# Kernel tuning notes

Hardware: AMD Instinct MI355X
Metric: run time of the kernel (lower is better)

## Reference

```python
import jax, jax.numpy as jnp
import numpy as np

N = 100000
E = 1000000
HID = 64
EDGE_DIM = 32
N_STEPS = 4


def _gru_cell(x, h, W_ih, b_ih, W_hh, b_hh):
    # PyTorch GRUCell: gates ordered (r, z, n) along the 3*hidden axis
    gi = x @ W_ih.T + b_ih  # [N, 3H]
    gh = h @ W_hh.T + b_hh  # [N, 3H]
    i_r, i_z, i_n = jnp.split(gi, 3, axis=-1)
    h_r, h_z, h_n = jnp.split(gh, 3, axis=-1)
    r = jax.nn.sigmoid(i_r + h_r)
    z = jax.nn.sigmoid(i_z + h_z)
    n = jnp.tanh(i_n + r * h_n)
    return (1.0 - z) * n + z * h


def setup_inputs() -> dict:
    key = jax.random.key(0)
    ks = jax.random.split(key, 12)
    s = 0.05
    h = jax.random.normal(ks[0], (N, HID), dtype=jnp.float32)
    edge_attr = jax.random.normal(ks[1], (E, EDGE_DIM), dtype=jnp.float32)
    edge_index = jax.random.randint(ks[2], (2, E), 0, N, dtype=jnp.int64)
    # msg_nn: Linear(edge_dim->hid), ReLU, Linear(hid->hid)
    W1 = jax.random.normal(ks[3], (HID, EDGE_DIM), dtype=jnp.float32) * s
    b1 = jax.random.normal(ks[4], (HID,), dtype=jnp.float32) * s
    W2 = jax.random.normal(ks[5], (HID, HID), dtype=jnp.float32) * s
    b2 = jax.random.normal(ks[6], (HID,), dtype=jnp.float32) * s
    # GRUCell params
    W_ih = jax.random.normal(ks[7], (3 * HID, HID), dtype=jnp.float32) * s
    b_ih = jax.random.normal(ks[8], (3 * HID,), dtype=jnp.float32) * s
    W_hh = jax.random.normal(ks[9], (3 * HID, HID), dtype=jnp.float32) * s
    b_hh = jax.random.normal(ks[10], (3 * HID,), dtype=jnp.float32) * s
    return {"h": h, "edge_attr": edge_attr, "edge_index": edge_index,
            "W1": W1, "b1": b1, "W2": W2, "b2": b2,
            "W_ih": W_ih, "b_ih": b_ih, "W_hh": W_hh, "b_hh": b_hh}


def reference(h, edge_attr, edge_index, W1, b1, W2, b2, W_ih, b_ih, W_hh, b_hh):
    i, j = edge_index[0], edge_index[1]
    # msg_nn(edge_attr) is independent of the step, so compute it once (same math)
    msg_base = jax.nn.relu(edge_attr @ W1.T + b1) @ W2.T + b2  # [E, HID]
    for _ in range(N_STEPS):
        msg = msg_base * h[j]                                   # gather + elemwise
        agg = jax.ops.segment_sum(msg, i, num_segments=N)       # scatter-add ('add' aggr)
        h = _gru_cell(agg, h, W_ih, b_ih, W_hh, b_hh)
    return h
```

## Files before the change

kernel.cpp:

```cpp
#include <hip/hip_runtime.h>
#include <hip/hip_bf16.h>

#define HID 64
#define EDIM 32
#define NSTEPS 4

__device__ __forceinline__ float bf2f(unsigned short u) {
    union { unsigned u32; float f; } x; x.u32 = ((unsigned)u) << 16; return x.f;
}
__device__ __forceinline__ unsigned short f2bf(float f) {
    union { float f; unsigned u; } x; x.f = f;
    unsigned r = x.u + 0x7fff + ((x.u >> 16) & 1);
    return (unsigned short)(r >> 16);
}
__device__ __forceinline__ float fast_sigmoid(float x) {
    return __builtin_amdgcn_rcpf(1.f + __expf(-x));
}
__device__ __forceinline__ float fast_tanh(float x) {
    return 1.f - 2.f * __builtin_amdgcn_rcpf(__expf(2.f * x) + 1.f);
}

__global__ __launch_bounds__(256) void k_msg_base(
    const float* __restrict__ edge_attr,
    const float* __restrict__ W1, const float* __restrict__ b1,
    const float* __restrict__ W2, const float* __restrict__ b2,
    unsigned short* __restrict__ msg, int E)
{
    __shared__ unsigned short smem[256 * 72];
    const int t = threadIdx.x;
    const int e = blockIdx.x * 256 + t;

    if (e < E) {
        float ea[EDIM];
        const float4* eap = reinterpret_cast<const float4*>(edge_attr + (size_t)e * EDIM);
        #pragma unroll
        for (int q = 0; q < EDIM / 4; ++q) {
            float4 v = eap[q];
            ea[q * 4 + 0] = v.x; ea[q * 4 + 1] = v.y;
            ea[q * 4 + 2] = v.z; ea[q * 4 + 3] = v.w;
        }

        float hid[HID];
        #pragma unroll
        for (int k = 0; k < HID; ++k) {
            float acc = b1[k];
            #pragma unroll
            for (int c = 0; c < EDIM; ++c) acc += ea[c] * W1[k * EDIM + c];
            hid[k] = acc > 0.f ? acc : 0.f;
        }

        for (int oc = 0; oc < HID; oc += 4) {
            float a0 = b2[oc + 0], a1 = b2[oc + 1], a2 = b2[oc + 2], a3 = b2[oc + 3];
            #pragma unroll
            for (int c = 0; c < HID; ++c) {
                float hv = hid[c];
                a0 += hv * W2[(oc + 0) * HID + c];
                a1 += hv * W2[(oc + 1) * HID + c];
                a2 += hv * W2[(oc + 2) * HID + c];
                a3 += hv * W2[(oc + 3) * HID + c];
            }
            smem[t * 72 + oc + 0] = f2bf(a0);
            smem[t * 72 + oc + 1] = f2bf(a1);
            smem[t * 72 + oc + 2] = f2bf(a2);
            smem[t * 72 + oc + 3] = f2bf(a3);
        }
    }
    __syncthreads();

    const size_t base = (size_t)blockIdx.x * 256 * HID;
    #pragma unroll
    for (int k = 0; k < 16; ++k) {
        int flat  = k * 256 + t;
        int e_loc = flat >> 4;
        int c4    = (flat & 15) * 4;
        if (blockIdx.x * 256 + e_loc < E) {
            ushort4 v = *reinterpret_cast<const ushort4*>(smem + e_loc * 72 + c4);
            *reinterpret_cast<ushort4*>(msg + base + (size_t)flat * 4) = v;
        }
    }
}

__global__ __launch_bounds__(256) void k_scatter(
    const unsigned* __restrict__ msg2, const float* __restrict__ h,
    const int* __restrict__ ei, unsigned* __restrict__ agg2, int E)
{
    size_t gid = (size_t)blockIdx.x * 256 + threadIdx.x;
    int e  = (int)(gid >> 5);
    int c2 = (int)(gid & 31);
    if (e >= E) return;
    int dst = ei[e];
    int src = ei[E + e];
    unsigned m = msg2[(size_t)e * 32 + c2];
    float2 hv = *reinterpret_cast<const float2*>(h + (size_t)src * HID + c2 * 2);
    float p0 = bf2f((unsigned short)(m & 0xffffu)) * hv.x;
    float p1 = bf2f((unsigned short)(m >> 16))     * hv.y;
    unsigned pk = (unsigned)f2bf(p0) | ((unsigned)f2bf(p1) << 16);
    unsigned* addr = agg2 + (size_t)dst * 32 + c2;
    asm volatile("global_atomic_pk_add_bf16 %0, %1, off" :: "v"(addr), "v"(pk) : "memory");
}

__global__ __launch_bounds__(256) void k_gru(
    const unsigned* __restrict__ agg2, float* __restrict__ h,
    const float* __restrict__ W_ih, const float* __restrict__ b_ih,
    const float* __restrict__ W_hh, const float* __restrict__ b_hh, int N)
{
    const int lane = threadIdx.x & 63;
    const int p = __builtin_amdgcn_readfirstlane(threadIdx.x >> 6);
    const int n = blockIdx.x * 64 + lane;
    const bool act = (n < N);

    float a[HID], hh[HID];
    if (act) {
        const uint4* ap = reinterpret_cast<const uint4*>(agg2 + (size_t)n * 32);
        #pragma unroll
        for (int q = 0; q < 8; ++q) {
            uint4 v = ap[q];
            a[q * 8 + 0] = bf2f((unsigned short)(v.x & 0xffffu));
            a[q * 8 + 1] = bf2f((unsigned short)(v.x >> 16));
            a[q * 8 + 2] = bf2f((unsigned short)(v.y & 0xffffu));
            a[q * 8 + 3] = bf2f((unsigned short)(v.y >> 16));
            a[q * 8 + 4] = bf2f((unsigned short)(v.z & 0xffffu));
            a[q * 8 + 5] = bf2f((unsigned short)(v.z >> 16));
            a[q * 8 + 6] = bf2f((unsigned short)(v.w & 0xffffu));
            a[q * 8 + 7] = bf2f((unsigned short)(v.w >> 16));
        }
        const float4* hp = reinterpret_cast<const float4*>(h + (size_t)n * HID);
        #pragma unroll
        for (int q = 0; q < 16; ++q) {
            float4 v = hp[q];
            hh[q * 4 + 0] = v.x; hh[q * 4 + 1] = v.y;
            hh[q * 4 + 2] = v.z; hh[q * 4 + 3] = v.w;
        }
    }
    __syncthreads();
    if (!act) return;

    float out[16];
    for (int kk = 0; kk < 16; ++kk) {
        const int k = p * 16 + kk;
        float ir = b_ih[k], iz = b_ih[HID + k], inn = b_ih[2 * HID + k];
        float hr = b_hh[k], hz = b_hh[HID + k], hnn = b_hh[2 * HID + k];
        #pragma unroll
        for (int c = 0; c < HID; ++c) {
            float av = a[c], hv = hh[c];
            ir  += av * W_ih[(0 * HID + k) * HID + c];
            iz  += av * W_ih[(1 * HID + k) * HID + c];
            inn += av * W_ih[(2 * HID + k) * HID + c];
            hr  += hv * W_hh[(0 * HID + k) * HID + c];
            hz  += hv * W_hh[(1 * HID + k) * HID + c];
            hnn += hv * W_hh[(2 * HID + k) * HID + c];
        }
        float r = fast_sigmoid(ir + hr);
        float z = fast_sigmoid(iz + hz);
        float nn = fast_tanh(inn + r * hnn);
        out[kk] = (1.f - z) * nn + z * hh[k];
    }

    float4* op = reinterpret_cast<float4*>(h + (size_t)n * HID + p * 16);
    #pragma unroll
    for (int q = 0; q < 4; ++q) {
        float4 o;
        o.x = out[q * 4 + 0]; o.y = out[q * 4 + 1];
        o.z = out[q * 4 + 2]; o.w = out[q * 4 + 3];
        op[q] = o;
    }
}

extern "C" void kernel_launch(void* const* d_in, const int* in_sizes, int n_in,
                              void* d_out, int out_size, void* d_ws, size_t ws_size,
                              hipStream_t stream) {
    const float* h_in      = (const float*)d_in[0];
    const float* edge_attr = (const float*)d_in[1];
    const int*   ei        = (const int*)d_in[2];
    const float* W1        = (const float*)d_in[3];
    const float* b1        = (const float*)d_in[4];
    const float* W2        = (const float*)d_in[5];
    const float* b2        = (const float*)d_in[6];
    const float* W_ih      = (const float*)d_in[7];
    const float* b_ih      = (const float*)d_in[8];
    const float* W_hh      = (const float*)d_in[9];
    const float* b_hh      = (const float*)d_in[10];

    const int N = in_sizes[0] / HID;
    const int E = in_sizes[1] / EDIM;

    float* h = (float*)d_out;
    unsigned short* msg = (unsigned short*)d_ws;
    unsigned* agg2 = (unsigned*)((char*)d_ws + (size_t)E * HID * sizeof(unsigned short));

    hipMemcpyAsync(h, h_in, (size_t)N * HID * sizeof(float),
                   hipMemcpyDeviceToDevice, stream);

    k_msg_base<<<(E + 255) / 256, 256, 0, stream>>>(edge_attr, W1, b1, W2, b2, msg, E);

    for (int s = 0; s < NSTEPS; ++s) {
        hipMemsetAsync(agg2, 0, (size_t)N * 32 * sizeof(unsigned), stream);
        size_t total = (size_t)E * 32;
        k_scatter<<<(unsigned)((total + 255) / 256), 256, 0, stream>>>(
            (const unsigned*)msg, h, ei, agg2, E);
        k_gru<<<(N + 63) / 64, 256, 0, stream>>>(agg2, h, W_ih, b_ih, W_hh, b_hh, N);
    }
}
```

Measured before the change: 2.279 ms.

## Replace atomic bf16 scatter with CSR-sorted gather aggregation

Builds a CSR structure by destination node each call (histogram, three-pass scan, atomic fill) and writes the per-edge message base in destination-sorted order. Each step then aggregates with one wavefront per node, reading contiguous messages and gathered source features, and accumulates in fp32 instead of doing bf16 packed atomics. This removes the per-step memset and atomic contention and improves accumulation precision. In exchange it adds preprocessing kernels and scattered writes in the message kernel, and a full wavefront per node may idle on low-degree nodes.

```diff
diff --git a/kernel.cpp b/kernel.cpp
--- a/kernel.cpp
+++ b/kernel.cpp
@@ -20,17 +20,89 @@
     return 1.f - 2.f * __builtin_amdgcn_rcpf(__expf(2.f * x) + 1.f);
 }
 
+__global__ __launch_bounds__(256) void k_hist(
+    const int* __restrict__ ei, int* __restrict__ cnt, int E)
+{
+    int e = blockIdx.x * 256 + threadIdx.x;
+    if (e >= E) return;
+    atomicAdd(&cnt[ei[e]], 1);
+}
+
+__global__ __launch_bounds__(256) void k_scan1(
+    const int* __restrict__ cnt, int* __restrict__ tmp,
+    int* __restrict__ partials, int N)
+{
+    __shared__ int s[256];
+    int tid = threadIdx.x;
+    int i = blockIdx.x * 256 + tid;
+    int v = (i < N) ? cnt[i] : 0;
+    s[tid] = v;
+    __syncthreads();
+    #pragma unroll
+    for (int off = 1; off < 256; off <<= 1) {
+        int t = (tid >= off) ? s[tid - off] : 0;
+        __syncthreads();
+        s[tid] += t;
+        __syncthreads();
+    }
+    if (i < N) tmp[i] = s[tid] - v;
+    if (tid == 255) partials[blockIdx.x] = s[255];
+}
+
+__global__ __launch_bounds__(512) void k_scan2(int* __restrict__ partials, int nb)
+{
+    __shared__ int s[512];
+    int tid = threadIdx.x;
+    int v = (tid < nb) ? partials[tid] : 0;
+    s[tid] = v;
+    __syncthreads();
+    #pragma unroll
+    for (int off = 1; off < 512; off <<= 1) {
+        int t = (tid >= off) ? s[tid - off] : 0;
+        __syncthreads();
+        s[tid] += t;
+        __syncthreads();
+    }
+    if (tid < nb) partials[tid] = s[tid] - v;
+}
+
+__global__ __launch_bounds__(256) void k_scan3(
+    const int* __restrict__ tmp, const int* __restrict__ partials,
+    int* __restrict__ row_ptr, int N, int E)
+{
+    int i = blockIdx.x * 256 + threadIdx.x;
+    if (i < N) row_ptr[i] = tmp[i] + partials[i >> 8];
+    if (i == 0) row_ptr[N] = E;
+}
+
+__global__ __launch_bounds__(256) void k_fill(
+    const int* __restrict__ ei, int* __restrict__ cursor,
+    int* __restrict__ posmap, int* __restrict__ src_perm, int E)
+{
+    int e = blockIdx.x * 256 + threadIdx.x;
+    if (e >= E) return;
+    int dst = ei[e];
+    int src = ei[E + e];
+    int pos = atomicAdd(&cursor[dst], 1);
+    posmap[e] = pos;
+    src_perm[pos] = src;
+}
+
 __global__ __launch_bounds__(256) void k_msg_base(
     const float* __restrict__ edge_attr,
     const float* __restrict__ W1, const float* __restrict__ b1,
     const float* __restrict__ W2, const float* __restrict__ b2,
-    unsigned short* __restrict__ msg, int E)
+    const int* __restrict__ posmap,
+    unsigned short* __restrict__ msg_perm, int E)
 {
     __shared__ unsigned short smem[256 * 72];
+    __shared__ int spos[256];
     const int t = threadIdx.x;
     const int e = blockIdx.x * 256 + t;
 
     if (e < E) {
+        spos[t] = posmap[e];
+
         float ea[EDIM];
         const float4* eap = reinterpret_cast<const float4*>(edge_attr + (size_t)e * EDIM);
         #pragma unroll
@@ -67,40 +139,41 @@
     }
     __syncthreads();
 
-    const size_t base = (size_t)blockIdx.x * 256 * HID;
-    #pragma unroll
-    for (int k = 0; k < 16; ++k) {
-        int flat  = k * 256 + t;
-        int e_loc = flat >> 4;
-        int c4    = (flat & 15) * 4;
+    #pragma unroll
+    for (int it = 0; it < 8; ++it) {
+        int flat  = it * 256 + t;
+        int e_loc = flat >> 3;
+        int c8    = (flat & 7) * 8;
         if (blockIdx.x * 256 + e_loc < E) {
-            ushort4 v = *reinterpret_cast<const ushort4*>(smem + e_loc * 72 + c4);
-            *reinterpret_cast<ushort4*>(msg + base + (size_t)flat * 4) = v;
-        }
-    }
-}
-
-__global__ __launch_bounds__(256) void k_scatter(
-    const unsigned* __restrict__ msg2, const float* __restrict__ h,
-    const int* __restrict__ ei, unsigned* __restrict__ agg2, int E)
-{
-    size_t gid = (size_t)blockIdx.x * 256 + threadIdx.x;
-    int e  = (int)(gid >> 5);
-    int c2 = (int)(gid & 31);
-    if (e >= E) return;
-    int dst = ei[e];
-    int src = ei[E + e];
-    unsigned m = msg2[(size_t)e * 32 + c2];
-    float2 hv = *reinterpret_cast<const float2*>(h + (size_t)src * HID + c2 * 2);
-    float p0 = bf2f((unsigned short)(m & 0xffffu)) * hv.x;
-    float p1 = bf2f((unsigned short)(m >> 16))     * hv.y;
-    unsigned pk = (unsigned)f2bf(p0) | ((unsigned)f2bf(p1) << 16);
-    unsigned* addr = agg2 + (size_t)dst * 32 + c2;
-    asm volatile("global_atomic_pk_add_bf16 %0, %1, off" :: "v"(addr), "v"(pk) : "memory");
+            uint4 v = *reinterpret_cast<const uint4*>(smem + e_loc * 72 + c8);
+            size_t dst = (size_t)spos[e_loc] * HID + c8;
+            *reinterpret_cast<uint4*>(msg_perm + dst) = v;
+        }
+    }
+}
+
+__global__ __launch_bounds__(256) void k_agg(
+    const unsigned short* __restrict__ msg_perm, const float* __restrict__ h,
+    const int* __restrict__ row_ptr, const int* __restrict__ src_perm,
+    float* __restrict__ agg, int N)
+{
+    int wid  = blockIdx.x * 4 + (threadIdx.x >> 6);
+    int lane = threadIdx.x & 63;
+    if (wid >= N) return;
+    int beg = row_ptr[wid];
+    int end = row_ptr[wid + 1];
+    float acc = 0.f;
+    for (int k = beg; k < end; ++k) {
+        int s = __builtin_amdgcn_readfirstlane(src_perm[k]);
+        float m  = bf2f(msg_perm[(size_t)k * HID + lane]);
+        float hv = h[(size_t)s * HID + lane];
+        acc += m * hv;
+    }
+    agg[(size_t)wid * HID + lane] = acc;
 }
 
 __global__ __launch_bounds__(256) void k_gru(
-    const unsigned* __restrict__ agg2, float* __restrict__ h,
+    const float* __restrict__ agg, float* __restrict__ h,
     const float* __restrict__ W_ih, const float* __restrict__ b_ih,
     const float* __restrict__ W_hh, const float* __restrict__ b_hh, int N)
 {
@@ -111,25 +184,16 @@
 
     float a[HID], hh[HID];
     if (act) {
-        const uint4* ap = reinterpret_cast<const uint4*>(agg2 + (size_t)n * 32);
-        #pragma unroll
-        for (int q = 0; q < 8; ++q) {
-            uint4 v = ap[q];
-            a[q * 8 + 0] = bf2f((unsigned short)(v.x & 0xffffu));
-            a[q * 8 + 1] = bf2f((unsigned short)(v.x >> 16));
-            a[q * 8 + 2] = bf2f((unsigned short)(v.y & 0xffffu));
-            a[q * 8 + 3] = bf2f((unsigned short)(v.y >> 16));
-            a[q * 8 + 4] = bf2f((unsigned short)(v.z & 0xffffu));
-            a[q * 8 + 5] = bf2f((unsigned short)(v.z >> 16));
-            a[q * 8 + 6] = bf2f((unsigned short)(v.w & 0xffffu));
-            a[q * 8 + 7] = bf2f((unsigned short)(v.w >> 16));
-        }
+        const float4* ap = reinterpret_cast<const float4*>(agg + (size_t)n * HID);
         const float4* hp = reinterpret_cast<const float4*>(h + (size_t)n * HID);
         #pragma unroll
         for (int q = 0; q < 16; ++q) {
-            float4 v = hp[q];
-            hh[q * 4 + 0] = v.x; hh[q * 4 + 1] = v.y;
-            hh[q * 4 + 2] = v.z; hh[q * 4 + 3] = v.w;
+            float4 v = ap[q];
+            a[q * 4 + 0] = v.x; a[q * 4 + 1] = v.y;
+            a[q * 4 + 2] = v.z; a[q * 4 + 3] = v.w;
+            float4 w = hp[q];
+            hh[q * 4 + 0] = w.x; hh[q * 4 + 1] = w.y;
+            hh[q * 4 + 2] = w.z; hh[q * 4 + 3] = w.w;
         }
     }
     __syncthreads();
@@ -183,21 +247,39 @@
 
     const int N = in_sizes[0] / HID;
     const int E = in_sizes[1] / EDIM;
+    const int NB = (N + 255) / 256;
 
     float* h = (float*)d_out;
-    unsigned short* msg = (unsigned short*)d_ws;
-    unsigned* agg2 = (unsigned*)((char*)d_ws + (size_t)E * HID * sizeof(unsigned short));
+
+    char* base = (char*)d_ws;
+    unsigned short* msg_perm = (unsigned short*)base;
+    base += (size_t)E * HID * sizeof(unsigned short);
+    float* agg = (float*)base;       base += (size_t)N * HID * sizeof(float);
+    int* row_ptr = (int*)base;       base += (size_t)(N + 1) * sizeof(int);
+    int* cursor  = (int*)base;       base += (size_t)N * sizeof(int);
+    int* cnt     = (int*)base;       base += (size_t)N * sizeof(int);
+    int* tmp     = (int*)base;       base += (size_t)N * sizeof(int);
+    int* partials= (int*)base;       base += 512 * sizeof(int);
+    int* posmap  = (int*)base;       base += (size_t)E * sizeof(int);
+    int* src_perm= (int*)base;
 
     hipMemcpyAsync(h, h_in, (size_t)N * HID * sizeof(float),
                    hipMemcpyDeviceToDevice, stream);
 
-    k_msg_base<<<(E + 255) / 256, 256, 0, stream>>>(edge_attr, W1, b1, W2, b2, msg, E);
+    hipMemsetAsync(cnt, 0, (size_t)N * sizeof(int), stream);
+    k_hist <<<(E + 255) / 256, 256, 0, stream>>>(ei, cnt, E);
+    k_scan1<<<NB, 256, 0, stream>>>(cnt, tmp, partials, N);
+    k_scan2<<<1, 512, 0, stream>>>(partials, NB);
+    k_scan3<<<NB, 256, 0, stream>>>(tmp, partials, row_ptr, N, E);
+    hipMemcpyAsync(cursor, row_ptr, (size_t)N * sizeof(int),
+                   hipMemcpyDeviceToDevice, stream);
+    k_fill <<<(E + 255) / 256, 256, 0, stream>>>(ei, cursor, posmap, src_perm, E);
+
+    k_msg_base<<<(E + 255) / 256, 256, 0, stream>>>(
+        edge_attr, W1, b1, W2, b2, posmap, msg_perm, E);
 
     for (int s = 0; s < NSTEPS; ++s) {
-        hipMemsetAsync(agg2, 0, (size_t)N * 32 * sizeof(unsigned), stream);
-        size_t total = (size_t)E * 32;
-        k_scatter<<<(unsigned)((total + 255) / 256), 256, 0, stream>>>(
-            (const unsigned*)msg, h, ei, agg2, E);
-        k_gru<<<(N + 63) / 64, 256, 0, stream>>>(agg2, h, W_ih, b_ih, W_hh, b_hh, N);
-    }
-}
+        k_agg<<<(N + 3) / 4, 256, 0, stream>>>(msg_perm, h, row_ptr, src_perm, agg, N);
+        k_gru<<<(N + 63) / 64, 256, 0, stream>>>(agg, h, W_ih, b_ih, W_hh, b_hh, N);
+    }
+}
```

Measured after the change: 1.992 ms. 1.14x faster.
